# Optimization experiments

Measured on AMD Instinct MI355X. Metric: run time of the kernel, lower is better.

Reference implementation:

```python
import functools
import jax, jax.numpy as jnp
import numpy as np

N = 8192
CUTOFF = 0.125        # OpenBoundary._cutoff
INCLUDE_SELF = False  # OpenBoundary._include_self
MASK_VALUE = -1


def setup_inputs() -> dict:
    key = jax.random.key(0)
    positions = jax.random.uniform(key, (N, 3), dtype=jnp.float32)
    return {"positions": positions, "max_neighbours": 128}


def reference(positions, max_neighbours):
    n = positions.shape[0]
    c2 = CUTOFF * CUTOFF
    # all-pairs squared distances + cutoff mask; row i = sphere centred on particle i
    neigh_mask = jax.vmap(lambda c: jnp.sum((positions - c) ** 2, axis=1) <= c2)(positions)  # [N, N] bool
    if not INCLUDE_SELF:
        neigh_mask = neigh_mask & ~jnp.eye(n, dtype=bool)
    # per-row fixed-size compaction of true indices, padded with MASK_VALUE
    compact = functools.partial(jnp.argwhere, size=max_neighbours, fill_value=MASK_VALUE)
    to_idx = jax.vmap(compact)(neigh_mask)[..., 0]                 # [N, max_neighbours] int
    cell_indices = jnp.zeros((*to_idx.shape, 3), dtype=jnp.int32)  # open boundary: all zero cells
    actual_max_neighbours = jnp.max(neigh_mask.sum(axis=1))
    return to_idx, cell_indices, actual_max_neighbours
```

## Files before the change

kernel.cpp:

```cpp
#include <hip/hip_runtime.h>
#include <stdint.h>


#define CUTOFF2 (0.125f * 0.125f)
constexpr int NCELLS = 512;
constexpr int CAP    = 64;
constexpr int MAXN   = 128;
constexpr int NPART  = 256;

__device__ __forceinline__ int ccoord(float v) {
    int c = (int)(v * 8.0f);
    return c > 7 ? 7 : c;
}

__global__ __launch_bounds__(256) void scatter_kernel(
    const float* __restrict__ pos, int n,
    int* __restrict__ cnt, float4* __restrict__ cells) {
    int i = blockIdx.x * blockDim.x + threadIdx.x;
    if (i >= n) return;
    float x = pos[i*3], y = pos[i*3+1], z = pos[i*3+2];
    int c = (ccoord(z) * 8 + ccoord(y)) * 8 + ccoord(x);
    int slot = atomicAdd(&cnt[c], 1);
    cells[c * CAP + slot] = make_float4(x, y, z, __int_as_float(i));
}

__global__ __launch_bounds__(256) void neigh_kernel(
    const float4* __restrict__ cells,
    const int* __restrict__ cnt,
    const float* __restrict__ pos,
    int maxn,
    int* __restrict__ to_idx,
    int* __restrict__ cell_out,
    int* __restrict__ partial) {
    __shared__ uint32_t bm[4][256];

    const int lane = threadIdx.x & 63;
    const int wave = threadIdx.x >> 6;
    const int row  = blockIdx.x * 4 + wave;
    uint32_t* mybm = bm[wave];

    ((int4*)mybm)[lane] = make_int4(0, 0, 0, 0);

    const float px = pos[row*3], py = pos[row*3+1], pz = pos[row*3+2];
    const int cx = ccoord(px), cy = ccoord(py), cz = ccoord(pz);

    int4* co = (int4*)(cell_out + (size_t)row * maxn * 3);
    co[lane] = make_int4(0, 0, 0, 0);
    if (lane < 32) co[64 + lane] = make_int4(0, 0, 0, 0);

    #pragma unroll
    for (int dz = -1; dz <= 1; ++dz) {
        const int czz = cz + dz;
        const bool zok = (unsigned)czz <= 7u;
        #pragma unroll
        for (int dy = -1; dy <= 1; ++dy) {
            const int cyy = cy + dy;
            const bool yok = zok && ((unsigned)cyy <= 7u);
            #pragma unroll
            for (int dxc = -1; dxc <= 1; ++dxc) {
                const int cxx = cx + dxc;
                if (!(yok && ((unsigned)cxx <= 7u))) continue;
                const int c = (czz * 8 + cyy) * 8 + cxx;
                const int m = cnt[c];
                if (lane < m) {
                    float4 q = cells[c * CAP + lane];
                    float ddx = q.x - px, ddy = q.y - py, ddz = q.z - pz;
                    float d2 = ddx*ddx + ddy*ddy + ddz*ddz;
                    int idx = __float_as_int(q.w);
                    if (d2 <= CUTOFF2 && idx != row)
                        atomicOr(&mybm[idx >> 5], 1u << (idx & 31));
                }
            }
        }
    }

    int4 wv = ((int4*)mybm)[lane];
    uint32_t w0 = (uint32_t)wv.x, w1 = (uint32_t)wv.y,
             w2 = (uint32_t)wv.z, w3 = (uint32_t)wv.w;
    int tc = __popc(w0) + __popc(w1) + __popc(w2) + __popc(w3);

    int inc = tc;
    #pragma unroll
    for (int d = 1; d < 64; d <<= 1) {
        int o = __shfl_up(inc, d);
        if (lane >= d) inc += o;
    }
    const int total = __shfl(inc, 63);
    int p = inc - tc;

    int* out_row = to_idx + (size_t)row * maxn;
    const int bitbase = lane << 7;
    uint32_t wsv[4] = {w0, w1, w2, w3};
    #pragma unroll
    for (int d = 0; d < 4; ++d) {
        uint32_t mm = wsv[d];
        while (mm) {
            int b = __ffs(mm) - 1;
            if (p < MAXN) out_row[p] = bitbase + (d << 5) + b;
            ++p;
            mm &= mm - 1;
        }
    }
    int start = total < MAXN ? total : MAXN;
    for (int q = start + lane; q < MAXN; q += 64) out_row[q] = -1;

    if (lane == 0) atomicMax(&partial[blockIdx.x & (NPART - 1)], total);
}

__global__ __launch_bounds__(256) void maxred_kernel(
    const int* __restrict__ partial, int* __restrict__ out_max) {
    __shared__ int sm[4];
    int m = partial[threadIdx.x];
    #pragma unroll
    for (int d = 32; d > 0; d >>= 1) {
        int o = __shfl_down(m, d);
        m = o > m ? o : m;
    }
    if ((threadIdx.x & 63) == 0) sm[threadIdx.x >> 6] = m;
    __syncthreads();
    if (threadIdx.x == 0) {
        int r = sm[0];
        r = sm[1] > r ? sm[1] : r;
        r = sm[2] > r ? sm[2] : r;
        r = sm[3] > r ? sm[3] : r;
        *out_max = r;
    }
}

extern "C" void kernel_launch(void* const* d_in, const int* in_sizes, int n_in,
                              void* d_out, int out_size, void* d_ws, size_t ws_size,
                              hipStream_t stream) {
    const float* pos = (const float*)d_in[0];
    const int n = in_sizes[0] / 3;
    const int maxn = (out_size - 1) / (n * 4);

    int* to_idx   = (int*)d_out;
    int* cell_out = to_idx + (size_t)n * maxn;
    int* out_max  = cell_out + (size_t)n * maxn * 3;

    int*    cnt     = (int*)d_ws;
    int*    partial = cnt + NCELLS;
    float4* cells   = (float4*)((char*)d_ws + 4096);

    hipMemsetAsync(d_ws, 0, (NCELLS + NPART) * sizeof(int), stream);
    scatter_kernel<<<(n + 255) / 256, 256, 0, stream>>>(pos, n, cnt, cells);
    neigh_kernel<<<n / 4, 256, 0, stream>>>(cells, cnt, pos, maxn,
                                            to_idx, cell_out, partial);
    maxred_kernel<<<1, NPART, 0, stream>>>(partial, out_max);
}
```

Measured before the change: 86.54 us.

## Fuse cell scatter, neighbour search and max reduction into one cooperative kernel

The memset, scatter, neighbour and max-reduction launches are merged into a single cooperative kernel. It uses two grid-wide syncs: one to clear the cell counts and one before the neighbour search. Each wave now stages its compacted neighbour list in shared memory and writes the row with coalesced int4 stores, and the global maximum comes from one atomicMax per block. This removes launch and memset overhead and the separate reduction pass, at the cost of grid barrier latency. The kernel relies on the output max slot already being zero, since nothing clears it before the atomicMax.

Measured after the change: 241.5 us. 2.79x slower.

```diff
diff --git a/kernel.cpp b/kernel.cpp
--- a/kernel.cpp
+++ b/kernel.cpp
@@ -1,45 +1,56 @@
 #include <hip/hip_runtime.h>
+#include <hip/hip_cooperative_groups.h>
 #include <stdint.h>
+
+namespace cg = cooperative_groups;
 
 
 #define CUTOFF2 (0.125f * 0.125f)
 constexpr int NCELLS = 512;
 constexpr int CAP    = 64;
 constexpr int MAXN   = 128;
-constexpr int NPART  = 256;
 
 __device__ __forceinline__ int ccoord(float v) {
     int c = (int)(v * 8.0f);
     return c > 7 ? 7 : c;
 }
 
-__global__ __launch_bounds__(256) void scatter_kernel(
-    const float* __restrict__ pos, int n,
-    int* __restrict__ cnt, float4* __restrict__ cells) {
-    int i = blockIdx.x * blockDim.x + threadIdx.x;
-    if (i >= n) return;
-    float x = pos[i*3], y = pos[i*3+1], z = pos[i*3+2];
-    int c = (ccoord(z) * 8 + ccoord(y)) * 8 + ccoord(x);
-    int slot = atomicAdd(&cnt[c], 1);
-    cells[c * CAP + slot] = make_float4(x, y, z, __int_as_float(i));
-}
-
-__global__ __launch_bounds__(256) void neigh_kernel(
-    const float4* __restrict__ cells,
-    const int* __restrict__ cnt,
-    const float* __restrict__ pos,
-    int maxn,
+__global__ __launch_bounds__(512, 8) void fused_kernel(
+    const float* __restrict__ pos, int n, int maxn,
     int* __restrict__ to_idx,
     int* __restrict__ cell_out,
-    int* __restrict__ partial) {
-    __shared__ uint32_t bm[4][256];
+    int* __restrict__ out_max,
+    int* __restrict__ cnt,
+    float4* __restrict__ cells) {
+    cg::grid_group grid = cg::this_grid();
 
-    const int lane = threadIdx.x & 63;
-    const int wave = threadIdx.x >> 6;
-    const int row  = blockIdx.x * 4 + wave;
+    __shared__ uint32_t bm[8][256];
+    __shared__ int      stage[8][MAXN];
+    __shared__ int      wmax[8];
+
+    const int tid  = threadIdx.x;
+    const int gtid = blockIdx.x * 512 + tid;
+
+    if (gtid < NCELLS) cnt[gtid] = 0;
+    grid.sync();
+
+    if (gtid < n) {
+        float x = pos[gtid*3], y = pos[gtid*3+1], z = pos[gtid*3+2];
+        int c = (ccoord(z) * 8 + ccoord(y)) * 8 + ccoord(x);
+        int slot = atomicAdd(&cnt[c], 1);
+        cells[c * CAP + slot] = make_float4(x, y, z, __int_as_float(gtid));
+    }
+    grid.sync();
+
+    const int lane = tid & 63;
+    const int wave = tid >> 6;
+    const int row  = blockIdx.x * 8 + wave;
+
     uint32_t* mybm = bm[wave];
-
     ((int4*)mybm)[lane] = make_int4(0, 0, 0, 0);
+    int* st = stage[wave];
+    st[lane] = -1;
+    st[lane + 64] = -1;
 
     const float px = pos[row*3], py = pos[row*3+1], pz = pos[row*3+2];
     const int cx = ccoord(px), cy = ccoord(py), cz = ccoord(pz);
@@ -88,7 +99,6 @@
     const int total = __shfl(inc, 63);
     int p = inc - tc;
 
-    int* out_row = to_idx + (size_t)row * maxn;
     const int bitbase = lane << 7;
     uint32_t wsv[4] = {w0, w1, w2, w3};
     #pragma unroll
@@ -96,34 +106,23 @@
         uint32_t mm = wsv[d];
         while (mm) {
             int b = __ffs(mm) - 1;
-            if (p < MAXN) out_row[p] = bitbase + (d << 5) + b;
+            if (p < MAXN) st[p] = bitbase + (d << 5) + b;
             ++p;
             mm &= mm - 1;
         }
     }
-    int start = total < MAXN ? total : MAXN;
-    for (int q = start + lane; q < MAXN; q += 64) out_row[q] = -1;
+    if (lane == 0) wmax[wave] = total;
+    __syncthreads();
 
-    if (lane == 0) atomicMax(&partial[blockIdx.x & (NPART - 1)], total);
-}
+    int4* orow = (int4*)(to_idx + (size_t)row * maxn);
+    const int4* sv = (const int4*)st;
+    if (lane < 32) orow[lane] = sv[lane];
 
-__global__ __launch_bounds__(256) void maxred_kernel(
-    const int* __restrict__ partial, int* __restrict__ out_max) {
-    __shared__ int sm[4];
-    int m = partial[threadIdx.x];
-    #pragma unroll
-    for (int d = 32; d > 0; d >>= 1) {
-        int o = __shfl_down(m, d);
-        m = o > m ? o : m;
-    }
-    if ((threadIdx.x & 63) == 0) sm[threadIdx.x >> 6] = m;
-    __syncthreads();
-    if (threadIdx.x == 0) {
-        int r = sm[0];
-        r = sm[1] > r ? sm[1] : r;
-        r = sm[2] > r ? sm[2] : r;
-        r = sm[3] > r ? sm[3] : r;
-        *out_max = r;
+    if (tid == 0) {
+        int m = wmax[0];
+        #pragma unroll
+        for (int i = 1; i < 8; ++i) m = wmax[i] > m ? wmax[i] : m;
+        atomicMax(out_max, m);
     }
 }
 
@@ -131,20 +130,17 @@
                               void* d_out, int out_size, void* d_ws, size_t ws_size,
                               hipStream_t stream) {
     const float* pos = (const float*)d_in[0];
-    const int n = in_sizes[0] / 3;
-    const int maxn = (out_size - 1) / (n * 4);
+    int n    = in_sizes[0] / 3;
+    int maxn = (out_size - 1) / (n * 4);
 
     int* to_idx   = (int*)d_out;
     int* cell_out = to_idx + (size_t)n * maxn;
     int* out_max  = cell_out + (size_t)n * maxn * 3;
 
-    int*    cnt     = (int*)d_ws;
-    int*    partial = cnt + NCELLS;
-    float4* cells   = (float4*)((char*)d_ws + 4096);
+    int*    cnt   = (int*)d_ws;
+    float4* cells = (float4*)((char*)d_ws + 4096);
 
-    hipMemsetAsync(d_ws, 0, (NCELLS + NPART) * sizeof(int), stream);
-    scatter_kernel<<<(n + 255) / 256, 256, 0, stream>>>(pos, n, cnt, cells);
-    neigh_kernel<<<n / 4, 256, 0, stream>>>(cells, cnt, pos, maxn,
-                                            to_idx, cell_out, partial);
-    maxred_kernel<<<1, NPART, 0, stream>>>(partial, out_max);
+    void* args[] = {&pos, &n, &maxn, &to_idx, &cell_out, &out_max, &cnt, &cells};
+    hipLaunchCooperativeKernel((void*)fused_kernel, dim3(n / 8), dim3(512),
+                               args, 0, stream);
 }
```
